# Performance work log

Measured on AMD Instinct MI355X. Metric: run time of the kernel, lower is better.

Reference implementation:

```python
import jax, jax.numpy as jnp
import numpy as np

D_SUMMARY = 128
N_LAYERS = 24
N_HEADS = 16
D_HEAD = 64
HIDDEN = 512
ACTIVE_MIN = 12
ROT = 16
THETA = 10000.0
B, P = 16, 128
L_ACT = N_LAYERS - ACTIVE_MIN
OUT_DIM = N_HEADS * 2 * D_HEAD


def setup_inputs() -> dict:
    key = jax.random.key(0)
    k1, k2, k3, k4, k5, k6 = jax.random.split(key, 6)
    summary_stack = jax.random.normal(k1, (B, P, D_SUMMARY), jnp.float32)
    positions = jnp.sort(jax.random.randint(k2, (P,), 0, 8192))
    s1 = 1.0 / np.sqrt(D_SUMMARY)
    s2 = 1.0 / np.sqrt(HIDDEN)
    W1 = jax.random.uniform(k3, (L_ACT, D_SUMMARY, HIDDEN), jnp.float32, -s1, s1)
    b1 = jax.random.uniform(k4, (L_ACT, HIDDEN), jnp.float32, -s1, s1)
    W2 = jax.random.uniform(k5, (L_ACT, HIDDEN, OUT_DIM), jnp.float32, -s2, s2)
    b2 = jax.random.uniform(k6, (L_ACT, OUT_DIM), jnp.float32, -s2, s2)
    return {"summary_stack": summary_stack, "positions": positions,
            "W1": W1, "b1": b1, "W2": W2, "b2": b2}


def reference(summary_stack, positions, W1, b1, W2, b2):
    # Batched 2-layer MLP across all active layers (grouped GEMM)
    h = jax.nn.relu(jnp.einsum('bps,lsh->lbph', summary_stack, W1) + b1[:, None, None, :])
    kv = jnp.einsum('lbph,lho->lbpo', h, W2) + b2[:, None, None, :]
    kv = kv.reshape(L_ACT, B, P, N_HEADS, 2, D_HEAD)
    k = jnp.transpose(kv[..., 0, :], (0, 1, 3, 2, 4))  # (L,B,H,P,D)
    v = jnp.transpose(kv[..., 1, :], (0, 1, 3, 2, 4))
    # RoPE on first ROT dims of K
    inv_freq = 1.0 / (THETA ** (jnp.arange(0, ROT, 2, dtype=jnp.float32) / ROT))
    freqs = positions.astype(jnp.float32)[:, None] * inv_freq[None, :]  # (P, ROT//2)
    emb = jnp.concatenate([freqs, freqs], axis=-1)  # (P, ROT)
    cos, sin = jnp.cos(emb), jnp.sin(emb)
    k_rot, k_pass = k[..., :ROT], k[..., ROT:]
    rot_half = jnp.concatenate([-k_rot[..., ROT // 2:], k_rot[..., :ROT // 2]], axis=-1)
    k_emb = k_rot * cos + rot_half * sin
    k = jnp.concatenate([k_emb, k_pass], axis=-1)
    # Inactive layers get zero K/V
    zeros = jnp.zeros((ACTIVE_MIN, B, N_HEADS, P, D_HEAD), k.dtype)
    k_all = jnp.concatenate([zeros, k], axis=0)
    v_all = jnp.concatenate([zeros, v], axis=0)
    return jnp.stack([k_all, v_all], axis=1)  # (n_layers, 2, B, H, P, D)
```

## Files before the change

kernel.cpp:

```cpp
#include <hip/hip_runtime.h>
#include <hip/hip_bf16.h>

#define L_ACT   12
#define BDIM    16
#define PDIM    128
#define DSUM    128
#define HID     512
#define ODIM    2048
#define NHEAD   16
#define DHEAD   64
#define MROWS   2048

typedef short short8 __attribute__((ext_vector_type(8)));
typedef float f32x4  __attribute__((ext_vector_type(4)));

__device__ __forceinline__ void gload_lds16(const __hip_bfloat16* g, __hip_bfloat16* l) {
  __builtin_amdgcn_global_load_lds(
      (const __attribute__((address_space(1))) unsigned int*)g,
      (__attribute__((address_space(3))) unsigned int*)l, 16, 0, 0);
}

__global__ __launch_bounds__(256) void zerofill_kernel(f32x4* __restrict__ p, int n16) {
  int stride = gridDim.x * 256;
  for (int i = blockIdx.x * 256 + threadIdx.x; i < n16; i += stride)
    p[i] = {0.f, 0.f, 0.f, 0.f};
}

__global__ __launch_bounds__(256) void prep_small(
    const float* __restrict__ summary, const int* __restrict__ positions,
    const float* __restrict__ W1,
    __hip_bfloat16* __restrict__ A_bf, float* __restrict__ cs,
    __hip_bfloat16* __restrict__ W1T) {
  const int bid = blockIdx.x;
  const int tid = threadIdx.x;
  if (bid < 1024) {
    int i = bid * 256 + tid;
    A_bf[i] = __float2bfloat16(summary[i]);
    if (i < PDIM * 8) {
      int p = i >> 3, f = i & 7;
      double inv = pow(10000.0, -(double)f / 8.0);
      double ang = (double)positions[p] * inv;
      cs[i]        = (float)cos(ang);
      cs[1024 + i] = (float)sin(ang);
    }
  } else {
    __shared__ float t[32][33];
    int idx = bid - 1024;
    int bx = idx & 15, by = (idx >> 4) & 3, l = idx >> 6;
    int o0 = bx * 32, j0 = by * 32;
    int tx = tid & 31, ty = tid >> 5;
    const float* ip = W1 + (size_t)l * DSUM * HID;
#pragma unroll
    for (int r = 0; r < 32; r += 8)
      t[ty + r][tx] = ip[(size_t)(j0 + ty + r) * HID + o0 + tx];
    __syncthreads();
    __hip_bfloat16* op = W1T + (size_t)l * DSUM * HID;
#pragma unroll
    for (int r = 0; r < 32; r += 8)
      op[(size_t)(o0 + ty + r) * DSUM + j0 + tx] = __float2bfloat16(t[tx][ty + r]);
  }
}

__global__ __launch_bounds__(256) void gemm1_128(
    const __hip_bfloat16* __restrict__ Aall,
    const __hip_bfloat16* __restrict__ Ball,
    const float* __restrict__ bias,
    __hip_bfloat16* __restrict__ Hall,
    const float* __restrict__ W2,
    __hip_bfloat16* __restrict__ W2T,
    f32x4* __restrict__ zeroBase, int doZero) {
  const int KTOT = DSUM, NTOT = HID;
  __shared__ __hip_bfloat16 shbuf[17408];
  __hip_bfloat16* ldsA = shbuf;
  __hip_bfloat16* ldsB = shbuf + 8192;
  const int l    = blockIdx.z;
  const int n0   = blockIdx.x * 128;
  const int m0   = blockIdx.y * 128;
  const int tid  = threadIdx.x;
  const int wid  = tid >> 6;
  const int lane = tid & 63;
  const int wr = wid >> 1, wc = wid & 1;
  const __hip_bfloat16* A  = Aall;
  const __hip_bfloat16* Bt = Ball + (size_t)l * NTOT * KTOT;

  f32x4 acc[4][4];
#pragma unroll
  for (int m = 0; m < 4; ++m)
#pragma unroll
    for (int n = 0; n < 4; ++n)
      acc[m][n] = {0.f, 0.f, 0.f, 0.f};

  const int srowi = lane >> 3;
  const int sblk  = (lane & 7) ^ srowi;

  for (int kt = 0; kt < KTOT / 64; ++kt) {
    __syncthreads();
#pragma unroll
    for (int s = 0; s < 4; ++s) {
      int seg = wid * 4 + s;
      int row = seg * 8 + srowi;
      gload_lds16(A  + (size_t)(m0 + row) * KTOT + kt * 64 + sblk * 8, ldsA + seg * 512);
      gload_lds16(Bt + (size_t)(n0 + row) * KTOT + kt * 64 + sblk * 8, ldsB + seg * 512);
    }
    __syncthreads();
#pragma unroll
    for (int kk = 0; kk < 2; ++kk) {
      short8 af[4], bfr[4];
#pragma unroll
      for (int m = 0; m < 4; ++m) {
        int row = wr * 64 + m * 16 + (lane & 15);
        int off = (kk * 64 + (lane >> 4) * 16) ^ ((row & 7) << 4);
        af[m] = *(const short8*)((const char*)ldsA + row * 128 + off);
      }
#pragma unroll
      for (int n = 0; n < 4; ++n) {
        int row = wc * 64 + n * 16 + (lane & 15);
        int off = (kk * 64 + (lane >> 4) * 16) ^ ((row & 7) << 4);
        bfr[n] = *(const short8*)((const char*)ldsB + row * 128 + off);
      }
#pragma unroll
      for (int m = 0; m < 4; ++m)
#pragma unroll
        for (int n = 0; n < 4; ++n)
          acc[m][n] = __builtin_amdgcn_mfma_f32_16x16x32_bf16(af[m], bfr[n], acc[m][n], 0, 0, 0);
    }
  }

  const int bid = blockIdx.x + 4 * blockIdx.y + 64 * blockIdx.z;

  if (doZero) {
    const f32x4 z = {0.f, 0.f, 0.f, 0.f};
    f32x4* zp = zeroBase + (size_t)bid * 16384;
#pragma unroll
    for (int i = 0; i < 64; ++i)
      __builtin_nontemporal_store(z, zp + i * 256 + tid);
  }

  __syncthreads();
#pragma unroll
  for (int n = 0; n < 4; ++n) {
    int col = wc * 64 + n * 16 + (lane & 15);
    float bb = bias[l * NTOT + n0 + col];
#pragma unroll
    for (int m = 0; m < 4; ++m) {
      int rowb = wr * 64 + m * 16 + ((lane >> 4) << 2);
#pragma unroll
      for (int j = 0; j < 4; ++j) {
        float v = acc[m][n][j] + bb;
        v = v > 0.f ? v : 0.f;
        shbuf[(rowb + j) * 136 + col] = __float2bfloat16(v);
      }
    }
  }
  __syncthreads();
  {
    __hip_bfloat16* H = Hall + (size_t)l * MROWS * HID;
#pragma unroll
    for (int i = 0; i < 8; ++i) {
      int idx = i * 256 + tid;
      int row = idx >> 4, seg = idx & 15;
      short8 v = *(const short8*)(shbuf + row * 136 + seg * 8);
      *(short8*)(H + (size_t)(m0 + row) * HID + n0 + seg * 8) = v;
    }
  }

  {
    float* tb = (float*)shbuf;
    const int tx = tid & 31, ty = tid >> 5;
    const int tbase = bid * 16;
#pragma unroll 1
    for (int tt = 0; tt < 16; ++tt) {
      int t = tbase + tt;
      int lz = t >> 10, rem = t & 1023;
      int jt = rem >> 6, ot = rem & 63;
      int j0 = jt * 32, o0 = ot * 32;
      const float* ip = W2 + (size_t)lz * HID * ODIM;
      __hip_bfloat16* op = W2T + (size_t)lz * HID * ODIM;
      __syncthreads();
#pragma unroll
      for (int r = 0; r < 32; r += 8)
        tb[(ty + r) * 33 + tx] = ip[(size_t)(j0 + ty + r) * ODIM + o0 + tx];
      __syncthreads();
#pragma unroll
      for (int r = 0; r < 32; r += 8)
        op[(size_t)(o0 + ty + r) * HID + j0 + tx] = __float2bfloat16(tb[tx * 33 + ty + r]);
    }
  }
}

__global__ __launch_bounds__(512, 1) void gemm2_pipe(
    const __hip_bfloat16* __restrict__ Aall,
    const __hip_bfloat16* __restrict__ Ball,
    const float* __restrict__ bias,
    const float* __restrict__ cs,
    float* __restrict__ O) {
  __shared__ __hip_bfloat16 lds[4 * 16384];
  const int orig = blockIdx.x + 8 * blockIdx.y + 64 * blockIdx.z;
  const int nw   = (orig & 7) * 96 + (orig >> 3);
  const int bx   = nw & 7;
  const int by   = (nw >> 3) & 7;
  const int l    = nw >> 6;
  const int n0  = bx * 256;
  const int m0  = by * 256;
  const int tid = threadIdx.x;
  const int wid = tid >> 6, lane = tid & 63;
  const int wm  = wid >> 2, wn = wid & 3;
  const __hip_bfloat16* A  = Aall + (size_t)l * MROWS * HID;
  const __hip_bfloat16* Bt = Ball + (size_t)l * ODIM * HID;

  f32x4 acc[8][4];
#pragma unroll
  for (int m = 0; m < 8; ++m)
#pragma unroll
    for (int n = 0; n < 4; ++n)
      acc[m][n] = {0.f, 0.f, 0.f, 0.f};

  const int cidx0 = wid * 128 + lane;
  const int cidx1 = cidx0 + 64;
  const int r0 = cidx0 >> 2, c0 = (cidx0 & 3) ^ ((r0 >> 1) & 3);
  const int r1 = cidx1 >> 2, c1 = (cidx1 & 3) ^ ((r1 >> 1) & 3);

#define STAGE_A(slot, kt) do {                                                      \
    gload_lds16(A + (size_t)(m0 + r0) * HID + (kt) * 32 + c0 * 8,                   \
                lds + (slot) * 16384 + wid * 1024);                                 \
    gload_lds16(A + (size_t)(m0 + r1) * HID + (kt) * 32 + c1 * 8,                   \
                lds + (slot) * 16384 + wid * 1024 + 512);                           \
  } while (0)
#define STAGE_B(slot, kt) do {                                                      \
    gload_lds16(Bt + (size_t)(n0 + r0) * HID + (kt) * 32 + c0 * 8,                  \
                lds + (slot) * 16384 + 8192 + wid * 1024);                          \
    gload_lds16(Bt + (size_t)(n0 + r1) * HID + (kt) * 32 + c1 * 8,                  \
                lds + (slot) * 16384 + 8192 + wid * 1024 + 512);                    \
  } while (0)

  const int kq   = lane >> 4;
  const int rl15 = lane & 15;

#define LD_FRAG(dst, base, rr) do {                                                 \
    int r_ = (rr);                                                                  \
    int off_ = r_ * 64 + ((kq ^ ((r_ >> 1) & 3)) << 4);                             \
    dst = *(const short8*)((const char*)(base) + off_);                             \
  } while (0)

  STAGE_A(0, 0); STAGE_B(0, 0);
  STAGE_A(1, 1); STAGE_B(1, 1);
  STAGE_A(2, 2); STAGE_B(2, 2);
  asm volatile("s_waitcnt vmcnt(8)" ::: "memory");
  __builtin_amdgcn_s_barrier();

  const int NT = HID / 32;
  for (int t = 0; t < NT; ++t) {
    const __hip_bfloat16* sa = lds + (t & 3) * 16384;
    const __hip_bfloat16* sb = sa + 8192;
    short8 af[4], bfr[4];

#pragma unroll
    for (int n = 0; n < 4; ++n) LD_FRAG(bfr[n], sb, wn * 64 + n * 16 + rl15);
#pragma unroll
    for (int mi = 0; mi < 4; ++mi) LD_FRAG(af[mi], sa, wm * 128 + mi * 16 + rl15);
    if (t + 3 < NT) STAGE_A((t + 3) & 3, t + 3);
    __builtin_amdgcn_s_barrier();
    __builtin_amdgcn_s_setprio(1);
#pragma unroll
    for (int mi = 0; mi < 4; ++mi)
#pragma unroll
      for (int n = 0; n < 4; ++n)
        acc[mi][n] = __builtin_amdgcn_mfma_f32_16x16x32_bf16(af[mi], bfr[n], acc[mi][n], 0, 0, 0);
    __builtin_amdgcn_s_setprio(0);
    __builtin_amdgcn_s_barrier();

#pragma unroll
    for (int mi = 0; mi < 4; ++mi) LD_FRAG(af[mi], sa, wm * 128 + 64 + mi * 16 + rl15);
    if (t + 3 < NT) STAGE_B((t + 3) & 3, t + 3);
    __builtin_amdgcn_s_barrier();
    __builtin_amdgcn_s_setprio(1);
#pragma unroll
    for (int mi = 0; mi < 4; ++mi)
#pragma unroll
      for (int n = 0; n < 4; ++n)
        acc[4 + mi][n] = __builtin_amdgcn_mfma_f32_16x16x32_bf16(af[mi], bfr[n], acc[4 + mi][n], 0, 0, 0);
    __builtin_amdgcn_s_setprio(0);
    if (t < NT - 1) {
      if (t <= NT - 4)      asm volatile("s_waitcnt vmcnt(8)" ::: "memory");
      else if (t == NT - 3) asm volatile("s_waitcnt vmcnt(4)" ::: "memory");
      else                  asm volatile("s_waitcnt vmcnt(0)" ::: "memory");
    }
    __builtin_amdgcn_s_barrier();
  }
#undef STAGE_A
#undef STAGE_B
#undef LD_FRAG

  __syncthreads();
  const int head = bx * 2 + (wn >> 1);
  const int tkv  = wn & 1;
  const int bidx = by * 2 + wm;
  float* slab = O + ((((size_t)(l + L_ACT) * 2 + tkv) * BDIM + bidx) * NHEAD + head) * (PDIM * DHEAD);
  const bool ropeWave = (tkv == 0);

  float bb[4];
#pragma unroll
  for (int n = 0; n < 4; ++n) bb[n] = bias[l * ODIM + n0 + wn * 64 + n * 16 + rl15];

  float* Tw = (float*)lds + wid * 2080;

#pragma unroll
  for (int c = 0; c < 4; ++c) {
#pragma unroll
    for (int mh = 0; mh < 2; ++mh) {
      int mf = c * 2 + mh;
      int pl = mh * 16 + (lane >> 4) * 4;
#pragma unroll
      for (int n = 0; n < 4; ++n) {
#pragma unroll
        for (int j = 0; j < 4; ++j) {
          float v = acc[mf][n][j] + bb[n];
          if (ropeWave && n == 0) {
            float partner = __shfl_xor(v, 8);
            int p = c * 32 + pl + j;
            float cv = cs[p * 8 + (lane & 7)];
            float sv = cs[1024 + p * 8 + (lane & 7)];
            v = v * cv + (((lane & 15) < 8) ? -partner : partner) * sv;
          }
          Tw[(pl + j) * 65 + n * 16 + rl15] = v;
        }
      }
    }
#pragma unroll
    for (int it = 0; it < 8; ++it) {
      int pl = it * 4 + (lane >> 4);
      f32x4 vv = *(const f32x4*)(Tw + pl * 65 + rl15 * 4);
      __builtin_nontemporal_store(vv, (f32x4*)(slab + (size_t)(c * 32 + pl) * DHEAD + rl15 * 4));
    }
  }
}

extern "C" void kernel_launch(void* const* d_in, const int* in_sizes, int n_in,
                              void* d_out, int out_size, void* d_ws, size_t ws_size,
                              hipStream_t stream) {
  const float* summary   = (const float*)d_in[0];
  const int*   positions = (const int*)d_in[1];
  const float* W1 = (const float*)d_in[2];
  const float* b1 = (const float*)d_in[3];
  const float* W2 = (const float*)d_in[4];
  const float* b2 = (const float*)d_in[5];
  float* out = (float*)d_out;

  const size_t SCRATCH_BYTES = 52436992;
  const bool useWs = (ws_size >= SCRATCH_BYTES);
  char* sc = useWs ? (char*)d_ws : (char*)d_out;
  __hip_bfloat16* h_bf = (__hip_bfloat16*)sc;
  __hip_bfloat16* W2T  = (__hip_bfloat16*)(sc + 25165824);
  __hip_bfloat16* W1T  = (__hip_bfloat16*)(sc + 50331648);
  __hip_bfloat16* A_bf = (__hip_bfloat16*)(sc + 51904512);
  float*          cs   = (float*)(sc + 52428800);

  prep_small<<<1792, 256, 0, stream>>>(summary, positions, W1, A_bf, cs, W1T);

  gemm1_128<<<dim3(HID / 128, MROWS / 128, L_ACT), 256, 0, stream>>>(
      A_bf, W1T, b1, h_bf, W2, W2T, (f32x4*)d_out, useWs ? 1 : 0);
  gemm2_pipe<<<dim3(ODIM / 256, MROWS / 256, L_ACT), 512, 0, stream>>>(h_bf, W2T, b2, cs, out);

  if (!useWs)
    zerofill_kernel<<<2048, 256, 0, stream>>>((f32x4*)d_out, 12582912);
}
```

Baseline: 135.4 us.

## Fuse summary bf16 conversion into gemm1 and software-pipeline W2 transpose with zero-fill

Removes the separate summary-to-bf16 pass from the prep kernel, so gemm1 reads fp32 summary directly, converts it in registers and writes swizzled bf16 into LDS. The W2 transpose tail in gemm1 is double-buffered: the next tile's global loads are issued before the current tile is stored, and the output zero-fill stores are interleaved into those iterations instead of running as one up-front burst. This shrinks the prep kernel and overlaps load latency with stores, at the cost of gemm1 reading A from global 16 times redundantly (per N-tile/layer) with regular loads instead of async LDS loads.

```diff
diff --git a/kernel.cpp b/kernel.cpp
--- a/kernel.cpp
+++ b/kernel.cpp
@@ -11,6 +11,7 @@
 #define DHEAD   64
 #define MROWS   2048
 
+typedef short s16x4  __attribute__((ext_vector_type(4)));
 typedef short short8 __attribute__((ext_vector_type(8)));
 typedef float f32x4  __attribute__((ext_vector_type(4)));
 
@@ -20,23 +21,26 @@
       (__attribute__((address_space(3))) unsigned int*)l, 16, 0, 0);
 }
 
+__device__ __forceinline__ short f2bf(float x) {
+  __hip_bfloat16 h = __float2bfloat16(x);
+  return *reinterpret_cast<short*>(&h);
+}
+
 __global__ __launch_bounds__(256) void zerofill_kernel(f32x4* __restrict__ p, int n16) {
   int stride = gridDim.x * 256;
   for (int i = blockIdx.x * 256 + threadIdx.x; i < n16; i += stride)
     p[i] = {0.f, 0.f, 0.f, 0.f};
 }
 
-__global__ __launch_bounds__(256) void prep_small(
-    const float* __restrict__ summary, const int* __restrict__ positions,
-    const float* __restrict__ W1,
-    __hip_bfloat16* __restrict__ A_bf, float* __restrict__ cs,
-    __hip_bfloat16* __restrict__ W1T) {
+__global__ __launch_bounds__(256) void prep_tiny(
+    const int* __restrict__ positions, const float* __restrict__ W1,
+    float* __restrict__ cs, __hip_bfloat16* __restrict__ W1T) {
   const int bid = blockIdx.x;
   const int tid = threadIdx.x;
-  if (bid < 1024) {
-    int i = bid * 256 + tid;
-    A_bf[i] = __float2bfloat16(summary[i]);
-    if (i < PDIM * 8) {
+  if (bid == 768) {
+#pragma unroll
+    for (int q = 0; q < 4; ++q) {
+      int i = q * 256 + tid;
       int p = i >> 3, f = i & 7;
       double inv = pow(10000.0, -(double)f / 8.0);
       double ang = (double)positions[p] * inv;
@@ -45,8 +49,7 @@
     }
   } else {
     __shared__ float t[32][33];
-    int idx = bid - 1024;
-    int bx = idx & 15, by = (idx >> 4) & 3, l = idx >> 6;
+    int bx = bid & 15, by = (bid >> 4) & 3, l = bid >> 6;
     int o0 = bx * 32, j0 = by * 32;
     int tx = tid & 31, ty = tid >> 5;
     const float* ip = W1 + (size_t)l * DSUM * HID;
@@ -62,7 +65,7 @@
 }
 
 __global__ __launch_bounds__(256) void gemm1_128(
-    const __hip_bfloat16* __restrict__ Aall,
+    const float* __restrict__ summary,
     const __hip_bfloat16* __restrict__ Ball,
     const float* __restrict__ bias,
     __hip_bfloat16* __restrict__ Hall,
@@ -80,7 +83,6 @@
   const int wid  = tid >> 6;
   const int lane = tid & 63;
   const int wr = wid >> 1, wc = wid & 1;
-  const __hip_bfloat16* A  = Aall;
   const __hip_bfloat16* Bt = Ball + (size_t)l * NTOT * KTOT;
 
   f32x4 acc[4][4];
@@ -99,8 +101,17 @@
     for (int s = 0; s < 4; ++s) {
       int seg = wid * 4 + s;
       int row = seg * 8 + srowi;
-      gload_lds16(A  + (size_t)(m0 + row) * KTOT + kt * 64 + sblk * 8, ldsA + seg * 512);
       gload_lds16(Bt + (size_t)(n0 + row) * KTOT + kt * 64 + sblk * 8, ldsB + seg * 512);
+    }
+#pragma unroll
+    for (int j = 0; j < 8; ++j) {
+      int s = j * 256 + tid;
+      int r = s >> 4, g = s & 15;
+      f32x4 v = *(const f32x4*)(summary + (size_t)(m0 + r) * DSUM + kt * 64 + g * 4);
+      s16x4 w;
+      w[0] = f2bf(v[0]); w[1] = f2bf(v[1]); w[2] = f2bf(v[2]); w[3] = f2bf(v[3]);
+      int ch = g >> 1;
+      *(s16x4*)((char*)ldsA + r * 128 + ((ch ^ (r & 7)) << 4) + (g & 1) * 8) = w;
     }
     __syncthreads();
 #pragma unroll
@@ -128,14 +139,6 @@
 
   const int bid = blockIdx.x + 4 * blockIdx.y + 64 * blockIdx.z;
 
-  if (doZero) {
-    const f32x4 z = {0.f, 0.f, 0.f, 0.f};
-    f32x4* zp = zeroBase + (size_t)bid * 16384;
-#pragma unroll
-    for (int i = 0; i < 64; ++i)
-      __builtin_nontemporal_store(z, zp + i * 256 + tid);
-  }
-
   __syncthreads();
 #pragma unroll
   for (int n = 0; n < 4; ++n) {
@@ -165,26 +168,71 @@
   }
 
   {
-    float* tb = (float*)shbuf;
+    float* tb0 = (float*)shbuf;
+    float* tb1 = (float*)shbuf + 1056;
     const int tx = tid & 31, ty = tid >> 5;
     const int tbase = bid * 16;
+    const f32x4 z = {0.f, 0.f, 0.f, 0.f};
+    f32x4* zp = zeroBase + (size_t)bid * 16384;
+    float rvA0, rvA1, rvA2, rvA3, rvB0, rvB1, rvB2, rvB3;
+
+#define W2_LOAD(P, tt_) do {                                                \
+      int t_ = tbase + (tt_);                                               \
+      int lz_ = t_ >> 10, rem_ = t_ & 1023;                                 \
+      int j0_ = (rem_ >> 6) * 32, o0_ = (rem_ & 63) * 32;                   \
+      const float* ip_ = W2 + (size_t)lz_ * HID * ODIM                      \
+                       + (size_t)(j0_ + ty) * ODIM + o0_ + tx;              \
+      P##0 = ip_[0];                                                        \
+      P##1 = ip_[(size_t)8 * ODIM];                                         \
+      P##2 = ip_[(size_t)16 * ODIM];                                        \
+      P##3 = ip_[(size_t)24 * ODIM];                                        \
+    } while (0)
+
+#define W2_WRITE(buf, P) do {                                               \
+      (buf)[(ty +  0) * 33 + tx] = P##0;                                    \
+      (buf)[(ty +  8) * 33 + tx] = P##1;                                    \
+      (buf)[(ty + 16) * 33 + tx] = P##2;                                    \
+      (buf)[(ty + 24) * 33 + tx] = P##3;                                    \
+    } while (0)
+
+#define W2_STORE(buf, tt_) do {                                             \
+      int t_ = tbase + (tt_);                                               \
+      int lz_ = t_ >> 10, rem_ = t_ & 1023;                                 \
+      int j0_ = (rem_ >> 6) * 32, o0_ = (rem_ & 63) * 32;                   \
+      __hip_bfloat16* op_ = W2T + (size_t)lz_ * HID * ODIM;                 \
+      _Pragma("unroll")                                                     \
+      for (int r_ = 0; r_ < 4; ++r_)                                        \
+        op_[(size_t)(o0_ + ty + 8 * r_) * HID + j0_ + tx] =                 \
+            __float2bfloat16((buf)[tx * 33 + ty + 8 * r_]);                 \
+    } while (0)
+
+#define ZCHUNK(tt_) do { if (doZero) {                                      \
+      _Pragma("unroll")                                                     \
+      for (int q_ = 0; q_ < 4; ++q_)                                        \
+        __builtin_nontemporal_store(z, zp + ((tt_) * 4 + q_) * 256 + tid);  \
+    } } while (0)
+
+    W2_LOAD(rvA, 0);
+    W2_LOAD(rvB, 1);
+    W2_WRITE(tb0, rvA);
+    __syncthreads();
 #pragma unroll 1
-    for (int tt = 0; tt < 16; ++tt) {
-      int t = tbase + tt;
-      int lz = t >> 10, rem = t & 1023;
-      int jt = rem >> 6, ot = rem & 63;
-      int j0 = jt * 32, o0 = ot * 32;
-      const float* ip = W2 + (size_t)lz * HID * ODIM;
-      __hip_bfloat16* op = W2T + (size_t)lz * HID * ODIM;
+    for (int tt = 0; tt < 16; tt += 2) {
+      if (tt + 2 < 16) W2_LOAD(rvA, tt + 2);
+      W2_STORE(tb0, tt);
+      W2_WRITE(tb1, rvB);
+      ZCHUNK(tt);
       __syncthreads();
-#pragma unroll
-      for (int r = 0; r < 32; r += 8)
-        tb[(ty + r) * 33 + tx] = ip[(size_t)(j0 + ty + r) * ODIM + o0 + tx];
+      if (tt + 3 < 16) W2_LOAD(rvB, tt + 3);
+      W2_STORE(tb1, tt + 1);
+      if (tt + 2 < 16) W2_WRITE(tb0, rvA);
+      ZCHUNK(tt + 1);
       __syncthreads();
-#pragma unroll
-      for (int r = 0; r < 32; r += 8)
-        op[(size_t)(o0 + ty + r) * HID + j0 + tx] = __float2bfloat16(tb[tx * 33 + ty + r]);
-    }
+    }
+#undef W2_LOAD
+#undef W2_WRITE
+#undef W2_STORE
+#undef ZCHUNK
   }
 }
 
@@ -346,19 +394,18 @@
   const float* b2 = (const float*)d_in[5];
   float* out = (float*)d_out;
 
-  const size_t SCRATCH_BYTES = 52436992;
+  const size_t SCRATCH_BYTES = 25165824ULL + 25165824ULL + 1572864ULL + 8192ULL;
   const bool useWs = (ws_size >= SCRATCH_BYTES);
   char* sc = useWs ? (char*)d_ws : (char*)d_out;
   __hip_bfloat16* h_bf = (__hip_bfloat16*)sc;
   __hip_bfloat16* W2T  = (__hip_bfloat16*)(sc + 25165824);
   __hip_bfloat16* W1T  = (__hip_bfloat16*)(sc + 50331648);
-  __hip_bfloat16* A_bf = (__hip_bfloat16*)(sc + 51904512);
-  float*          cs   = (float*)(sc + 52428800);
-
-  prep_small<<<1792, 256, 0, stream>>>(summary, positions, W1, A_bf, cs, W1T);
+  float*          cs   = (float*)(sc + 51904512);
+
+  prep_tiny<<<769, 256, 0, stream>>>(positions, W1, cs, W1T);
 
   gemm1_128<<<dim3(HID / 128, MROWS / 128, L_ACT), 256, 0, stream>>>(
-      A_bf, W1T, b1, h_bf, W2, W2T, (f32x4*)d_out, useWs ? 1 : 0);
+      summary, W1T, b1, h_bf, W2, W2T, (f32x4*)d_out, useWs ? 1 : 0);
   gemm2_pipe<<<dim3(ODIM / 256, MROWS / 256, L_ACT), 512, 0, stream>>>(h_bf, W2T, b2, cs, out);
 
   if (!useWs)
```

After: 129.9 us. 4.0% less time.
